# Kernel optimization log

Measured on AMD Instinct MI355X. Metric: run time of the kernel, lower is better.

## Reference

```python
import jax, jax.numpy as jnp
import numpy as np
from jax import lax

T, B, K, H, L = 256, 64, 1024, 1024, 3

def setup_inputs() -> dict:
    key = jax.random.key(0)
    ks = jax.random.split(key, 6)
    x = jax.random.normal(ks[0], (T, B, K), dtype=jnp.float32)
    h0 = jax.random.normal(ks[1], (L, B, H), dtype=jnp.float32) * 0.1
    # xavier-ish / orthogonal-ish scale for stability
    w_ih = jax.random.normal(ks[2], (L, 3 * H, K), dtype=jnp.float32) * (1.0 / np.sqrt(K))
    w_hh = jax.random.normal(ks[3], (L, 3 * H, H), dtype=jnp.float32) * (1.0 / np.sqrt(H))
    b_ih = jnp.zeros((L, 3 * H), dtype=jnp.float32)
    b_hh = jnp.zeros((L, 3 * H), dtype=jnp.float32)
    return {"x": x, "h0": h0, "w_ih": w_ih, "w_hh": w_hh, "b_ih": b_ih, "b_hh": b_hh}

def _gru_layer(x_seq, h_init, wih, whh, bih, bhh):
    # x_seq: [T,B,Kin], h_init: [B,H], wih: [3H,Kin], whh: [3H,H]
    Hd = h_init.shape[-1]
    # precompute input-to-hidden projections for all timesteps in one GEMM
    gi = jnp.einsum('tbk,gk->tbg', x_seq, wih) + bih  # [T,B,3H]

    def step(h, gi_t):
        gh = h @ whh.T + bhh  # [B,3H]
        r = jax.nn.sigmoid(gi_t[:, :Hd] + gh[:, :Hd])
        z = jax.nn.sigmoid(gi_t[:, Hd:2 * Hd] + gh[:, Hd:2 * Hd])
        n = jnp.tanh(gi_t[:, 2 * Hd:] + r * gh[:, 2 * Hd:])
        h_new = (1.0 - z) * n + z * h
        return h_new, h_new

    h_last, outs = lax.scan(step, h_init, gi)
    return h_last, outs  # [B,H], [T,B,H]

def reference(x, h0, w_ih, w_hh, b_ih, b_hh):
    layer_in = x
    h_n = []
    for l in range(w_ih.shape[0]):
        h_last, layer_in = _gru_layer(layer_in, h0[l], w_ih[l], w_hh[l], b_ih[l], b_hh[l])
        h_n.append(h_last)
    return jnp.stack(h_n, axis=0)  # [L,B,H]
```

## Files before the change

kernel.cpp:

```cpp
#include <hip/hip_runtime.h>
#include <hip/hip_bf16.h>

typedef __attribute__((ext_vector_type(8))) short bf16x8;
typedef __attribute__((ext_vector_type(4))) float f32x4;

#define T_STEPS 256
#define BATCH   64
#define KDIM    1024
#define HDIM    1024
#define NGATE   3072
#define LAYERS  3
#define SLOTE   (BATCH * HDIM)
#define RING_SLOTS (T_STEPS + 1)
#define WSZ     (192L * 32 * 64 * 8)
#define FSTRIDE 4

#define LDS_BS_BYTES  65536
#define LDS_WIS_BYTES 65536
#define GI_PAR_FLOATS (3 * 64 * 20)
#define LDS_GI_BYTES  (2 * GI_PAR_FLOATS * 4)
#define LDS_CTRL_OFF  (LDS_BS_BYTES + LDS_WIS_BYTES + LDS_GI_BYTES)
#define LDS_TOTAL     (LDS_CTRL_OFF + 32)

#define MFMA16(a, b, c) __builtin_amdgcn_mfma_f32_16x16x32_bf16(a, b, c, 0, 0, 0)

__device__ __forceinline__ unsigned short f2b(float f) {
  union { float f; unsigned int u; } a; a.f = f;
  unsigned int u = a.u;
  unsigned int r = (u + 0x7FFFu + ((u >> 16) & 1u)) >> 16;
  return (unsigned short)r;
}
__device__ __forceinline__ void gload16(const void* gptr, void* ldsptr) {
  __builtin_amdgcn_global_load_lds(
      (const __attribute__((address_space(1))) unsigned int*)gptr,
      (__attribute__((address_space(3))) unsigned int*)ldsptr,
      16, 0, 0);
}

__global__ void f2b_kernel(const float* __restrict__ src,
                           unsigned short* __restrict__ dst, int n4) {
  int i = blockIdx.x * blockDim.x + threadIdx.x;
  if (i < n4) {
    float4 v = ((const float4*)src)[i];
    ushort4 o;
    o.x = f2b(v.x); o.y = f2b(v.y); o.z = f2b(v.z); o.w = f2b(v.w);
    ((ushort4*)dst)[i] = o;
  }
}

__global__ void swizzle_w(const float* __restrict__ w,
                          unsigned short* __restrict__ out) {
  long gid = (long)blockIdx.x * 256 + threadIdx.x;
  int lane = (int)(gid & 63);
  long rest = gid >> 6;
  int kc = (int)(rest & 31); rest >>= 5;
  int ntile = (int)(rest % 192); int l = (int)(rest / 192);
  int n  = ntile * 16 + (lane & 15);
  int k0 = kc * 32 + (lane >> 4) * 8;
  const float* src = w + (((long)l * NGATE + n) * KDIM + k0);
  unsigned short o[8];
#pragma unroll
  for (int j = 0; j < 8; j++) o[j] = f2b(src[j]);
  bf16x8 v = *(bf16x8*)o;
  *(bf16x8*)(out + gid * 8) = v;
}

__global__ __launch_bounds__(512, 2) void gru_fused(
    const unsigned short* __restrict__ xb,
    const unsigned short* __restrict__ wswhh,
    const unsigned short* __restrict__ wswih,
    const float* __restrict__ bih,
    const float* __restrict__ bhh,
    const float* __restrict__ h0,
    unsigned short* __restrict__ rings,
    float* __restrict__ hout,
    unsigned int* __restrict__ flags)
{
  extern __shared__ __align__(16) char smem[];
  unsigned short* Bs  = (unsigned short*)smem;
  unsigned short* Wis = (unsigned short*)(smem + LDS_BS_BYTES);
  float* gi_lds = (float*)(smem + LDS_BS_BYTES + LDS_WIS_BYTES);
  unsigned int* ctrl = (unsigned int*)(smem + LDS_CTRL_OFF);

  int l = blockIdx.x >> 6, g = blockIdx.x & 63;
  int tid = threadIdx.x, wave = tid >> 6, lane = tid & 63;
  int lg = lane >> 4;
  int rg = wave & 3;
  bool is_h = (wave < 4);
  int row = rg * 16 + (lane & 15);
  int cb  = g * 16 + lg * 4;

  const unsigned short* whh_l = wswhh + (size_t)l * WSZ;
  const unsigned short* wih_l = wswih + (size_t)l * WSZ;
  unsigned short* ring_l = rings + (size_t)l * RING_SLOTS * SLOTE;
  const unsigned short* prev_ring = rings + (size_t)(l - 1) * RING_SLOTS * SLOTE;
  unsigned int* fl = flags + (size_t)l * 64 * FSTRIDE;
  const unsigned int* fp = flags + (size_t)(l > 0 ? (l - 1) : 0) * 64 * FSTRIDE;

  if (tid < 8) ctrl[tid] = 0;

#pragma unroll
  for (int i = 0; i < 16; i++) {
    int p = wave * 16 + i;
    int gate = (p >> 5) & 1;
    int kc = p & 31;
    const unsigned short* src = (p < 64)
        ? whh_l + ((((long)gate * 64 + g) * 32 + kc) * 64 + lane) * 8
        : wih_l + ((((long)gate * 64 + g) * 32 + kc) * 64 + lane) * 8;
    unsigned short* dst = (p < 64)
        ? &Bs[(size_t)p * 512 + (size_t)lane * 8]
        : &Wis[(size_t)(p - 64) * 512 + (size_t)lane * 8];
    gload16(src, dst);
  }

  bf16x8 wn[32];
  {
    const unsigned short* base = is_h ? whh_l : wih_l;
#pragma unroll
    for (int kc = 0; kc < 32; kc++)
      wn[kc] = *(const bf16x8*)(base + ((((long)(2 * 64 + g)) * 32 + kc) * 64 + lane) * 8);
  }

  float br_[4], bz_[4], bi_n[4], bh_n[4];
  float h[4] = {0.f, 0.f, 0.f, 0.f};
  if (is_h) {
    const float* bh_l = bhh + l * NGATE;
    const float* bi_l = bih + l * NGATE;
    float4 bhr4 = *(const float4*)(bh_l + 0 * HDIM + cb);
    float4 bhz4 = *(const float4*)(bh_l + 1 * HDIM + cb);
    float4 bhn4 = *(const float4*)(bh_l + 2 * HDIM + cb);
    float4 bir4 = *(const float4*)(bi_l + 0 * HDIM + cb);
    float4 biz4 = *(const float4*)(bi_l + 1 * HDIM + cb);
    float4 bin4 = *(const float4*)(bi_l + 2 * HDIM + cb);
    br_[0] = bir4.x + bhr4.x; br_[1] = bir4.y + bhr4.y; br_[2] = bir4.z + bhr4.z; br_[3] = bir4.w + bhr4.w;
    bz_[0] = biz4.x + bhz4.x; bz_[1] = biz4.y + bhz4.y; bz_[2] = biz4.z + bhz4.z; bz_[3] = biz4.w + bhz4.w;
    bi_n[0] = bin4.x; bi_n[1] = bin4.y; bi_n[2] = bin4.z; bi_n[3] = bin4.w;
    bh_n[0] = bhn4.x; bh_n[1] = bhn4.y; bh_n[2] = bhn4.z; bh_n[3] = bhn4.w;

    float4 h4 = *(const float4*)(h0 + (size_t)l * SLOTE + (size_t)row * HDIM + cb);
    h[0] = h4.x; h[1] = h4.y; h[2] = h4.z; h[3] = h4.w;
    union { unsigned short us[4]; unsigned long long u; } pk;
#pragma unroll
    for (int r = 0; r < 4; r++) pk.us[r] = f2b(h[r]);
    unsigned short* slotT = ring_l + (size_t)T_STEPS * SLOTE;
    __hip_atomic_store((unsigned long long*)(slotT + (size_t)g * 1024 + (size_t)row * 16 + lg * 4),
                       pk.u, __ATOMIC_RELAXED, __HIP_MEMORY_SCOPE_AGENT);
  }

  auto xgemv = [&](int tt) {
    f32x4 air = {}, aiz = {}, ain = {};
    if (l == 0) {
      const unsigned short* xa_b = xb + (size_t)tt * SLOTE + (size_t)row * KDIM + lg * 8;
#pragma unroll
      for (int kb = 0; kb < 4; kb++) {
        bf16x8 xa[8];
#pragma unroll
        for (int j = 0; j < 8; j++)
          xa[j] = *(const bf16x8*)(xa_b + (size_t)(kb * 8 + j) * 32);
#pragma unroll
        for (int j = 0; j < 8; j++) {
          int kc = kb * 8 + j;
          bf16x8 wir = *(const bf16x8*)&Wis[(size_t)kc * 512 + (size_t)lane * 8];
          bf16x8 wiz = *(const bf16x8*)&Wis[(size_t)(32 + kc) * 512 + (size_t)lane * 8];
          air = MFMA16(wir, xa[j], air);
          aiz = MFMA16(wiz, xa[j], aiz);
          ain = MFMA16(wn[kc], xa[j], ain);
        }
      }
    } else {
      const unsigned short* xa_b = prev_ring + (size_t)(T_STEPS - 1 - tt) * SLOTE
                                   + (size_t)(lg >> 1) * 1024 + (size_t)row * 16 + (lg & 1) * 8;
#pragma unroll
      for (int kb = 0; kb < 4; kb++) {
        bf16x8 xa[8];
#pragma unroll
        for (int j = 0; j < 8; j++)
          xa[j] = *(const bf16x8*)(xa_b + (size_t)(kb * 8 + j) * 2048);
#pragma unroll
        for (int j = 0; j < 8; j++) {
          int kc = kb * 8 + j;
          bf16x8 wir = *(const bf16x8*)&Wis[(size_t)kc * 512 + (size_t)lane * 8];
          bf16x8 wiz = *(const bf16x8*)&Wis[(size_t)(32 + kc) * 512 + (size_t)lane * 8];
          air = MFMA16(wir, xa[j], air);
          aiz = MFMA16(wiz, xa[j], aiz);
          ain = MFMA16(wn[kc], xa[j], ain);
        }
      }
    }
    unsigned tgt = 4u * (unsigned)(tt >> 1);
    while (__hip_atomic_load(&ctrl[3 + (tt & 1)], __ATOMIC_ACQUIRE,
                             __HIP_MEMORY_SCOPE_WORKGROUP) < tgt) {}
    float* gp = gi_lds + (size_t)(tt & 1) * GI_PAR_FLOATS + (size_t)row * 20 + lg * 4;
    *(f32x4*)(gp + 0)    = air;
    *(f32x4*)(gp + 1280) = aiz;
    *(f32x4*)(gp + 2560) = ain;
    if (lane == 0)
      __hip_atomic_fetch_add(&ctrl[1 + (tt & 1)], 1u, __ATOMIC_RELEASE,
                             __HIP_MEMORY_SCOPE_WORKGROUP);
  };

  __syncthreads();
  if (tid == 0)
    __hip_atomic_store(&fl[g * FSTRIDE], 1u, __ATOMIC_RELAXED, __HIP_MEMORY_SCOPE_AGENT);

  if (is_h) {
    while (__hip_atomic_load(&fl[lane * FSTRIDE], __ATOMIC_RELAXED,
                             __HIP_MEMORY_SCOPE_AGENT) < 1u) {}
    asm volatile("" ::: "memory");
  } else {
    if (l > 0) {
      while (__hip_atomic_load(&fp[lane * FSTRIDE], __ATOMIC_RELAXED,
                               __HIP_MEMORY_SCOPE_AGENT) < 2u) {}
      asm volatile("" ::: "memory");
    }
    xgemv(0);
  }

#pragma unroll 1
  for (int t = 0; t < T_STEPS; t++) {
    if (is_h) {
      while (__hip_atomic_load(&ctrl[1 + (t & 1)], __ATOMIC_ACQUIRE,
                               __HIP_MEMORY_SCOPE_WORKGROUP)
             < 4u * (unsigned)((t >> 1) + 1)) {}
      const float* gp = gi_lds + (size_t)(t & 1) * GI_PAR_FLOATS + (size_t)row * 20 + lg * 4;
      f32x4 xir = *(const f32x4*)(gp + 0);
      f32x4 xiz = *(const f32x4*)(gp + 1280);
      f32x4 xin = *(const f32x4*)(gp + 2560);
      asm volatile("s_waitcnt lgkmcnt(0)" ::: "memory");
      __builtin_amdgcn_sched_barrier(0);
      if (lane == 0)
        __hip_atomic_fetch_add(&ctrl[3 + (t & 1)], 1u, __ATOMIC_RELEASE,
                               __HIP_MEMORY_SCOPE_WORKGROUP);

      const unsigned short* ha_b = ring_l + (size_t)(T_STEPS - t) * SLOTE
                                   + (size_t)(lg >> 1) * 1024 + (size_t)row * 16 + (lg & 1) * 8;
      f32x4 ahr = {}, ahz = {}, ahn = {};
#pragma unroll
      for (int kb = 0; kb < 4; kb++) {
        bf16x8 hh[8];
#pragma unroll
        for (int j = 0; j < 8; j++)
          hh[j] = *(const bf16x8*)(ha_b + (size_t)(kb * 8 + j) * 2048);
#pragma unroll
        for (int j = 0; j < 8; j++) {
          int kc = kb * 8 + j;
          bf16x8 whr = *(const bf16x8*)&Bs[(size_t)kc * 512 + (size_t)lane * 8];
          bf16x8 whz = *(const bf16x8*)&Bs[(size_t)(32 + kc) * 512 + (size_t)lane * 8];
          ahr = MFMA16(whr, hh[j], ahr);
          ahz = MFMA16(whz, hh[j], ahz);
          ahn = MFMA16(wn[kc], hh[j], ahn);
        }
      }

      unsigned short* hn = ring_l + (size_t)(T_STEPS - 1 - t) * SLOTE;
      union { unsigned short us[4]; unsigned long long u; } pk;
#pragma unroll
      for (int r = 0; r < 4; r++) {
        float xr = xir[r] + ahr[r] + br_[r];
        float xz = xiz[r] + ahz[r] + bz_[r];
        float rr = 1.0f / (1.0f + __expf(-xr));
        float zz = 1.0f / (1.0f + __expf(-xz));
        float xn = (xin[r] + bi_n[r]) + rr * (ahn[r] + bh_n[r]);
        float e2 = __expf(-2.0f * xn);
        float nn = (1.0f - e2) / (1.0f + e2);
        float hv = (1.0f - zz) * nn + zz * h[r];
        h[r] = hv;
        pk.us[r] = f2b(hv);
      }
      __hip_atomic_store((unsigned long long*)(hn + (size_t)g * 1024 + (size_t)row * 16 + lg * 4),
                         pk.u, __ATOMIC_RELAXED, __HIP_MEMORY_SCOPE_AGENT);
      if (t == T_STEPS - 1) {
        float4 o; o.x = h[0]; o.y = h[1]; o.z = h[2]; o.w = h[3];
        *(float4*)(hout + (size_t)l * SLOTE + (size_t)row * HDIM + cb) = o;
      }

      asm volatile("s_waitcnt vmcnt(0)" ::: "memory");
      if (lane == 0)
        __hip_atomic_fetch_add(&ctrl[0], 1u, __ATOMIC_RELEASE,
                               __HIP_MEMORY_SCOPE_WORKGROUP);
      if (wave == 0) {
        while (__hip_atomic_load(&ctrl[0], __ATOMIC_ACQUIRE,
                                 __HIP_MEMORY_SCOPE_WORKGROUP)
               < 4u * (unsigned)(t + 1)) {}
        asm volatile("" ::: "memory");
        if (tid == 0)
          __hip_atomic_store(&fl[g * FSTRIDE], (unsigned)(t + 2),
                             __ATOMIC_RELAXED, __HIP_MEMORY_SCOPE_AGENT);
      }
      if (t + 1 < T_STEPS) {
        while (__hip_atomic_load(&fl[lane * FSTRIDE], __ATOMIC_RELAXED,
                                 __HIP_MEMORY_SCOPE_AGENT) < (unsigned)(t + 2)) {}
        asm volatile("" ::: "memory");
      }
    } else if (t + 1 < T_STEPS) {
      if (l > 0) {
        while (__hip_atomic_load(&fp[lane * FSTRIDE], __ATOMIC_RELAXED,
                                 __HIP_MEMORY_SCOPE_AGENT) < (unsigned)(t + 3)) {}
        asm volatile("" ::: "memory");
      }
      xgemv(t + 1);
    }
  }
}

extern "C" void kernel_launch(void* const* d_in, const int* in_sizes, int n_in,
                              void* d_out, int out_size, void* d_ws, size_t ws_size,
                              hipStream_t stream) {
  const float* x   = (const float*)d_in[0];
  const float* h0  = (const float*)d_in[1];
  const float* wih = (const float*)d_in[2];
  const float* whh = (const float*)d_in[3];
  const float* bih = (const float*)d_in[4];
  const float* bhh = (const float*)d_in[5];
  float* out = (float*)d_out;

  char* p = (char*)d_ws;
  unsigned short* xb    = (unsigned short*)p; p += (size_t)T_STEPS * SLOTE * 2;
  unsigned short* wswhh = (unsigned short*)p; p += (size_t)LAYERS * WSZ * 2;
  unsigned short* wswih = (unsigned short*)p; p += (size_t)LAYERS * WSZ * 2;
  unsigned short* rings = (unsigned short*)p; p += (size_t)LAYERS * RING_SLOTS * SLOTE * 2;
  unsigned int*   flags = (unsigned int*)p;   p += 4096;

  static int attr_set = 0;
  if (!attr_set) {
    hipFuncSetAttribute((const void*)gru_fused,
                        hipFuncAttributeMaxDynamicSharedMemorySize, LDS_TOTAL);
    attr_set = 1;
  }

  hipMemsetAsync(flags, 0, 4096, stream);
  f2b_kernel<<<16384, 256, 0, stream>>>(x, xb, (T_STEPS * SLOTE) / 4);
  swizzle_w<<<4608, 256, 0, stream>>>(whh, wswhh);
  swizzle_w<<<4608, 256, 0, stream>>>(wih, wswih);

  gru_fused<<<LAYERS * 64, 512, LDS_TOTAL, stream>>>(
      xb, wswhh, wswih, bih, bhh, h0, rings, out, flags);
}
```

Baseline: 2.739 ms.

## Split batch into two independent half-streams to overlap cross-block sync with compute

The batch of 64 is split into two independent 32-row halves, each with its own ring buffer, flags and LDS gate-input double buffers. Each block drops from 512 to 256 threads: two h-waves process both halves in turn and two x-waves compute input projections for both halves. While one half waits on the grid-wide flag barrier, the other half's recurrent GEMV can proceed, which is meant to hide the per-timestep global synchronization latency. In exchange each block has half the waves, so the serial work per wave doubles, and there are twice as many flags to poll.

```diff
diff --git a/kernel.cpp b/kernel.cpp
--- a/kernel.cpp
+++ b/kernel.cpp
@@ -11,16 +11,17 @@
 #define NGATE   3072
 #define LAYERS  3
 #define SLOTE   (BATCH * HDIM)
+#define HSLOTE  (32 * 1024)
 #define RING_SLOTS (T_STEPS + 1)
 #define WSZ     (192L * 32 * 64 * 8)
 #define FSTRIDE 4
 
 #define LDS_BS_BYTES  65536
 #define LDS_WIS_BYTES 65536
-#define GI_PAR_FLOATS (3 * 64 * 20)
-#define LDS_GI_BYTES  (2 * GI_PAR_FLOATS * 4)
+#define GI_BUF_FLOATS (3 * 32 * 20)
+#define LDS_GI_BYTES  (4 * GI_BUF_FLOATS * 4)
 #define LDS_CTRL_OFF  (LDS_BS_BYTES + LDS_WIS_BYTES + LDS_GI_BYTES)
-#define LDS_TOTAL     (LDS_CTRL_OFF + 32)
+#define LDS_TOTAL     (LDS_CTRL_OFF + 64)
 
 #define MFMA16(a, b, c) __builtin_amdgcn_mfma_f32_16x16x32_bf16(a, b, c, 0, 0, 0)
 
@@ -65,7 +66,7 @@
   *(bf16x8*)(out + gid * 8) = v;
 }
 
-__global__ __launch_bounds__(512, 2) void gru_fused(
+__global__ __launch_bounds__(256, 1) void gru_fused(
     const unsigned short* __restrict__ xb,
     const unsigned short* __restrict__ wswhh,
     const unsigned short* __restrict__ wswih,
@@ -85,23 +86,30 @@
   int l = blockIdx.x >> 6, g = blockIdx.x & 63;
   int tid = threadIdx.x, wave = tid >> 6, lane = tid & 63;
   int lg = lane >> 4;
-  int rg = wave & 3;
-  bool is_h = (wave < 4);
-  int row = rg * 16 + (lane & 15);
-  int cb  = g * 16 + lg * 4;
+  bool is_h = (wave < 2);
+  int w = is_h ? wave : wave - 2;
+  int rh = w * 16 + (lane & 15);
+  int cb = g * 16 + lg * 4;
 
   const unsigned short* whh_l = wswhh + (size_t)l * WSZ;
   const unsigned short* wih_l = wswih + (size_t)l * WSZ;
-  unsigned short* ring_l = rings + (size_t)l * RING_SLOTS * SLOTE;
-  const unsigned short* prev_ring = rings + (size_t)(l - 1) * RING_SLOTS * SLOTE;
-  unsigned int* fl = flags + (size_t)l * 64 * FSTRIDE;
-  const unsigned int* fp = flags + (size_t)(l > 0 ? (l - 1) : 0) * 64 * FSTRIDE;
-
-  if (tid < 8) ctrl[tid] = 0;
-
-#pragma unroll
-  for (int i = 0; i < 16; i++) {
-    int p = wave * 16 + i;
+  unsigned short* ring_m[2];
+  const unsigned short* prev_m[2];
+  unsigned int* fl_m[2];
+  const unsigned int* fp_m[2];
+#pragma unroll
+  for (int m = 0; m < 2; m++) {
+    ring_m[m] = rings + (size_t)(l * 2 + m) * RING_SLOTS * HSLOTE;
+    prev_m[m] = rings + (size_t)((l > 0 ? l - 1 : 0) * 2 + m) * RING_SLOTS * HSLOTE;
+    fl_m[m] = flags + (size_t)(l * 2 + m) * 64 * FSTRIDE;
+    fp_m[m] = flags + (size_t)((l > 0 ? l - 1 : 0) * 2 + m) * 64 * FSTRIDE;
+  }
+
+  if (tid < 16) ctrl[tid] = 0;
+
+#pragma unroll
+  for (int i = 0; i < 32; i++) {
+    int p = wave + i * 4;
     int gate = (p >> 5) & 1;
     int kc = p & 31;
     const unsigned short* src = (p < 64)
@@ -122,7 +130,7 @@
   }
 
   float br_[4], bz_[4], bi_n[4], bh_n[4];
-  float h[4] = {0.f, 0.f, 0.f, 0.f};
+  float hS[2][4];
   if (is_h) {
     const float* bh_l = bhh + l * NGATE;
     const float* bi_l = bih + l * NGATE;
@@ -136,21 +144,23 @@
     bz_[0] = biz4.x + bhz4.x; bz_[1] = biz4.y + bhz4.y; bz_[2] = biz4.z + bhz4.z; bz_[3] = biz4.w + bhz4.w;
     bi_n[0] = bin4.x; bi_n[1] = bin4.y; bi_n[2] = bin4.z; bi_n[3] = bin4.w;
     bh_n[0] = bhn4.x; bh_n[1] = bhn4.y; bh_n[2] = bhn4.z; bh_n[3] = bhn4.w;
-
-    float4 h4 = *(const float4*)(h0 + (size_t)l * SLOTE + (size_t)row * HDIM + cb);
-    h[0] = h4.x; h[1] = h4.y; h[2] = h4.z; h[3] = h4.w;
-    union { unsigned short us[4]; unsigned long long u; } pk;
-#pragma unroll
-    for (int r = 0; r < 4; r++) pk.us[r] = f2b(h[r]);
-    unsigned short* slotT = ring_l + (size_t)T_STEPS * SLOTE;
-    __hip_atomic_store((unsigned long long*)(slotT + (size_t)g * 1024 + (size_t)row * 16 + lg * 4),
-                       pk.u, __ATOMIC_RELAXED, __HIP_MEMORY_SCOPE_AGENT);
-  }
-
-  auto xgemv = [&](int tt) {
+#pragma unroll
+    for (int m = 0; m < 2; m++) {
+      float4 h4 = *(const float4*)(h0 + (size_t)l * SLOTE + (size_t)(m * 32 + rh) * HDIM + cb);
+      hS[m][0] = h4.x; hS[m][1] = h4.y; hS[m][2] = h4.z; hS[m][3] = h4.w;
+      union { unsigned short us[4]; unsigned long long u; } pk;
+#pragma unroll
+      for (int r = 0; r < 4; r++) pk.us[r] = f2b(hS[m][r]);
+      unsigned short* slotT = ring_m[m] + (size_t)T_STEPS * HSLOTE;
+      __hip_atomic_store((unsigned long long*)(slotT + (size_t)g * 512 + (size_t)rh * 16 + lg * 4),
+                         pk.u, __ATOMIC_RELAXED, __HIP_MEMORY_SCOPE_AGENT);
+    }
+  }
+
+  auto xgemv = [&](int m, int tt) {
     f32x4 air = {}, aiz = {}, ain = {};
     if (l == 0) {
-      const unsigned short* xa_b = xb + (size_t)tt * SLOTE + (size_t)row * KDIM + lg * 8;
+      const unsigned short* xa_b = xb + (size_t)tt * SLOTE + (size_t)(m * 32 + rh) * KDIM + lg * 8;
 #pragma unroll
       for (int kb = 0; kb < 4; kb++) {
         bf16x8 xa[8];
@@ -168,14 +178,14 @@
         }
       }
     } else {
-      const unsigned short* xa_b = prev_ring + (size_t)(T_STEPS - 1 - tt) * SLOTE
-                                   + (size_t)(lg >> 1) * 1024 + (size_t)row * 16 + (lg & 1) * 8;
+      const unsigned short* xa_b = prev_m[m] + (size_t)(T_STEPS - 1 - tt) * HSLOTE
+                                   + (size_t)(lg >> 1) * 512 + (size_t)rh * 16 + (lg & 1) * 8;
 #pragma unroll
       for (int kb = 0; kb < 4; kb++) {
         bf16x8 xa[8];
 #pragma unroll
         for (int j = 0; j < 8; j++)
-          xa[j] = *(const bf16x8*)(xa_b + (size_t)(kb * 8 + j) * 2048);
+          xa[j] = *(const bf16x8*)(xa_b + (size_t)(kb * 8 + j) * 1024);
 #pragma unroll
         for (int j = 0; j < 8; j++) {
           int kc = kb * 8 + j;
@@ -187,118 +197,130 @@
         }
       }
     }
-    unsigned tgt = 4u * (unsigned)(tt >> 1);
-    while (__hip_atomic_load(&ctrl[3 + (tt & 1)], __ATOMIC_ACQUIRE,
-                             __HIP_MEMORY_SCOPE_WORKGROUP) < tgt) {}
-    float* gp = gi_lds + (size_t)(tt & 1) * GI_PAR_FLOATS + (size_t)row * 20 + lg * 4;
+    int p = tt & 1;
+    while (__hip_atomic_load(&ctrl[6 + m * 2 + p], __ATOMIC_ACQUIRE,
+                             __HIP_MEMORY_SCOPE_WORKGROUP) < 2u * (unsigned)(tt >> 1)) {}
+    float* gp = gi_lds + (size_t)(m * 2 + p) * GI_BUF_FLOATS + (size_t)rh * 20 + lg * 4;
     *(f32x4*)(gp + 0)    = air;
-    *(f32x4*)(gp + 1280) = aiz;
-    *(f32x4*)(gp + 2560) = ain;
+    *(f32x4*)(gp + 640)  = aiz;
+    *(f32x4*)(gp + 1280) = ain;
     if (lane == 0)
-      __hip_atomic_fetch_add(&ctrl[1 + (tt & 1)], 1u, __ATOMIC_RELEASE,
+      __hip_atomic_fetch_add(&ctrl[2 + m * 2 + p], 1u, __ATOMIC_RELEASE,
                              __HIP_MEMORY_SCOPE_WORKGROUP);
   };
 
   __syncthreads();
-  if (tid == 0)
-    __hip_atomic_store(&fl[g * FSTRIDE], 1u, __ATOMIC_RELAXED, __HIP_MEMORY_SCOPE_AGENT);
+  if (tid == 0) {
+    __hip_atomic_store(&fl_m[0][g * FSTRIDE], 1u, __ATOMIC_RELAXED, __HIP_MEMORY_SCOPE_AGENT);
+    __hip_atomic_store(&fl_m[1][g * FSTRIDE], 1u, __ATOMIC_RELAXED, __HIP_MEMORY_SCOPE_AGENT);
+  }
 
   if (is_h) {
-    while (__hip_atomic_load(&fl[lane * FSTRIDE], __ATOMIC_RELAXED,
-                             __HIP_MEMORY_SCOPE_AGENT) < 1u) {}
+#pragma unroll
+    for (int m = 0; m < 2; m++) {
+      while (__hip_atomic_load(&fl_m[m][lane * FSTRIDE], __ATOMIC_RELAXED,
+                               __HIP_MEMORY_SCOPE_AGENT) < 1u) {}
+    }
     asm volatile("" ::: "memory");
   } else {
     if (l > 0) {
-      while (__hip_atomic_load(&fp[lane * FSTRIDE], __ATOMIC_RELAXED,
-                               __HIP_MEMORY_SCOPE_AGENT) < 2u) {}
+#pragma unroll
+      for (int m = 0; m < 2; m++) {
+        while (__hip_atomic_load(&fp_m[m][lane * FSTRIDE], __ATOMIC_RELAXED,
+                                 __HIP_MEMORY_SCOPE_AGENT) < 2u) {}
+      }
       asm volatile("" ::: "memory");
     }
-    xgemv(0);
-  }
+    xgemv(0, 0);
+    xgemv(1, 0);
+  }
+
+  auto hsub = [&](int m, int t) {
+    if (t > 0) {
+      while (__hip_atomic_load(&fl_m[m][lane * FSTRIDE], __ATOMIC_RELAXED,
+                               __HIP_MEMORY_SCOPE_AGENT) < (unsigned)(t + 1)) {}
+      asm volatile("" ::: "memory");
+    }
+    const unsigned short* ha_b = ring_m[m] + (size_t)(T_STEPS - t) * HSLOTE
+                                 + (size_t)(lg >> 1) * 512 + (size_t)rh * 16 + (lg & 1) * 8;
+    bf16x8 ha[32];
+#pragma unroll
+    for (int kc = 0; kc < 32; kc++)
+      ha[kc] = *(const bf16x8*)(ha_b + (size_t)kc * 1024);
+
+    int p = t & 1;
+    while (__hip_atomic_load(&ctrl[2 + m * 2 + p], __ATOMIC_ACQUIRE,
+                             __HIP_MEMORY_SCOPE_WORKGROUP) < 2u * (unsigned)((t >> 1) + 1)) {}
+    const float* gp = gi_lds + (size_t)(m * 2 + p) * GI_BUF_FLOATS + (size_t)rh * 20 + lg * 4;
+    f32x4 xir = *(const f32x4*)(gp + 0);
+    f32x4 xiz = *(const f32x4*)(gp + 640);
+    f32x4 xin = *(const f32x4*)(gp + 1280);
+    asm volatile("s_waitcnt lgkmcnt(0)" ::: "memory");
+    __builtin_amdgcn_sched_barrier(0);
+    if (lane == 0)
+      __hip_atomic_fetch_add(&ctrl[6 + m * 2 + p], 1u, __ATOMIC_RELEASE,
+                             __HIP_MEMORY_SCOPE_WORKGROUP);
+
+    f32x4 ahr = {}, ahz = {}, ahn = {};
+#pragma unroll
+    for (int kc = 0; kc < 32; kc++) {
+      bf16x8 whr = *(const bf16x8*)&Bs[(size_t)kc * 512 + (size_t)lane * 8];
+      bf16x8 whz = *(const bf16x8*)&Bs[(size_t)(32 + kc) * 512 + (size_t)lane * 8];
+      ahr = MFMA16(whr, ha[kc], ahr);
+      ahz = MFMA16(whz, ha[kc], ahz);
+      ahn = MFMA16(wn[kc], ha[kc], ahn);
+    }
+
+    unsigned short* hn = ring_m[m] + (size_t)(T_STEPS - 1 - t) * HSLOTE;
+    union { unsigned short us[4]; unsigned long long u; } pk;
+#pragma unroll
+    for (int r = 0; r < 4; r++) {
+      float xr = xir[r] + ahr[r] + br_[r];
+      float xz = xiz[r] + ahz[r] + bz_[r];
+      float rr = 1.0f / (1.0f + __expf(-xr));
+      float zz = 1.0f / (1.0f + __expf(-xz));
+      float xn = (xin[r] + bi_n[r]) + rr * (ahn[r] + bh_n[r]);
+      float e2 = __expf(-2.0f * xn);
+      float nn = (1.0f - e2) / (1.0f + e2);
+      float hv = (1.0f - zz) * nn + zz * hS[m][r];
+      hS[m][r] = hv;
+      pk.us[r] = f2b(hv);
+    }
+    __hip_atomic_store((unsigned long long*)(hn + (size_t)g * 512 + (size_t)rh * 16 + lg * 4),
+                       pk.u, __ATOMIC_RELAXED, __HIP_MEMORY_SCOPE_AGENT);
+    if (t == T_STEPS - 1) {
+      float4 o; o.x = hS[m][0]; o.y = hS[m][1]; o.z = hS[m][2]; o.w = hS[m][3];
+      *(float4*)(hout + (size_t)l * SLOTE + (size_t)(m * 32 + rh) * HDIM + cb) = o;
+    }
+
+    asm volatile("s_waitcnt vmcnt(0)" ::: "memory");
+    if (lane == 0)
+      __hip_atomic_fetch_add(&ctrl[m], 1u, __ATOMIC_RELEASE, __HIP_MEMORY_SCOPE_WORKGROUP);
+    if (w == 0) {
+      while (__hip_atomic_load(&ctrl[m], __ATOMIC_ACQUIRE,
+                               __HIP_MEMORY_SCOPE_WORKGROUP) < 2u * (unsigned)(t + 1)) {}
+      asm volatile("" ::: "memory");
+      if (lane == 0)
+        __hip_atomic_store(&fl_m[m][g * FSTRIDE], (unsigned)(t + 2),
+                           __ATOMIC_RELAXED, __HIP_MEMORY_SCOPE_AGENT);
+    }
+  };
 
 #pragma unroll 1
   for (int t = 0; t < T_STEPS; t++) {
     if (is_h) {
-      while (__hip_atomic_load(&ctrl[1 + (t & 1)], __ATOMIC_ACQUIRE,
-                               __HIP_MEMORY_SCOPE_WORKGROUP)
-             < 4u * (unsigned)((t >> 1) + 1)) {}
-      const float* gp = gi_lds + (size_t)(t & 1) * GI_PAR_FLOATS + (size_t)row * 20 + lg * 4;
-      f32x4 xir = *(const f32x4*)(gp + 0);
-      f32x4 xiz = *(const f32x4*)(gp + 1280);
-      f32x4 xin = *(const f32x4*)(gp + 2560);
-      asm volatile("s_waitcnt lgkmcnt(0)" ::: "memory");
-      __builtin_amdgcn_sched_barrier(0);
-      if (lane == 0)
-        __hip_atomic_fetch_add(&ctrl[3 + (t & 1)], 1u, __ATOMIC_RELEASE,
-                               __HIP_MEMORY_SCOPE_WORKGROUP);
-
-      const unsigned short* ha_b = ring_l + (size_t)(T_STEPS - t) * SLOTE
-                                   + (size_t)(lg >> 1) * 1024 + (size_t)row * 16 + (lg & 1) * 8;
-      f32x4 ahr = {}, ahz = {}, ahn = {};
-#pragma unroll
-      for (int kb = 0; kb < 4; kb++) {
-        bf16x8 hh[8];
-#pragma unroll
-        for (int j = 0; j < 8; j++)
-          hh[j] = *(const bf16x8*)(ha_b + (size_t)(kb * 8 + j) * 2048);
-#pragma unroll
-        for (int j = 0; j < 8; j++) {
-          int kc = kb * 8 + j;
-          bf16x8 whr = *(const bf16x8*)&Bs[(size_t)kc * 512 + (size_t)lane * 8];
-          bf16x8 whz = *(const bf16x8*)&Bs[(size_t)(32 + kc) * 512 + (size_t)lane * 8];
-          ahr = MFMA16(whr, hh[j], ahr);
-          ahz = MFMA16(whz, hh[j], ahz);
-          ahn = MFMA16(wn[kc], hh[j], ahn);
+      hsub(0, t);
+      hsub(1, t);
+    } else if (t + 1 < T_STEPS) {
+#pragma unroll
+      for (int m = 0; m < 2; m++) {
+        if (l > 0) {
+          while (__hip_atomic_load(&fp_m[m][lane * FSTRIDE], __ATOMIC_RELAXED,
+                                   __HIP_MEMORY_SCOPE_AGENT) < (unsigned)(t + 3)) {}
+          asm volatile("" ::: "memory");
         }
+        xgemv(m, t + 1);
       }
-
-      unsigned short* hn = ring_l + (size_t)(T_STEPS - 1 - t) * SLOTE;
-      union { unsigned short us[4]; unsigned long long u; } pk;
-#pragma unroll
-      for (int r = 0; r < 4; r++) {
-        float xr = xir[r] + ahr[r] + br_[r];
-        float xz = xiz[r] + ahz[r] + bz_[r];
-        float rr = 1.0f / (1.0f + __expf(-xr));
-        float zz = 1.0f / (1.0f + __expf(-xz));
-        float xn = (xin[r] + bi_n[r]) + rr * (ahn[r] + bh_n[r]);
-        float e2 = __expf(-2.0f * xn);
-        float nn = (1.0f - e2) / (1.0f + e2);
-        float hv = (1.0f - zz) * nn + zz * h[r];
-        h[r] = hv;
-        pk.us[r] = f2b(hv);
-      }
-      __hip_atomic_store((unsigned long long*)(hn + (size_t)g * 1024 + (size_t)row * 16 + lg * 4),
-                         pk.u, __ATOMIC_RELAXED, __HIP_MEMORY_SCOPE_AGENT);
-      if (t == T_STEPS - 1) {
-        float4 o; o.x = h[0]; o.y = h[1]; o.z = h[2]; o.w = h[3];
-        *(float4*)(hout + (size_t)l * SLOTE + (size_t)row * HDIM + cb) = o;
-      }
-
-      asm volatile("s_waitcnt vmcnt(0)" ::: "memory");
-      if (lane == 0)
-        __hip_atomic_fetch_add(&ctrl[0], 1u, __ATOMIC_RELEASE,
-                               __HIP_MEMORY_SCOPE_WORKGROUP);
-      if (wave == 0) {
-        while (__hip_atomic_load(&ctrl[0], __ATOMIC_ACQUIRE,
-                                 __HIP_MEMORY_SCOPE_WORKGROUP)
-               < 4u * (unsigned)(t + 1)) {}
-        asm volatile("" ::: "memory");
-        if (tid == 0)
-          __hip_atomic_store(&fl[g * FSTRIDE], (unsigned)(t + 2),
-                             __ATOMIC_RELAXED, __HIP_MEMORY_SCOPE_AGENT);
-      }
-      if (t + 1 < T_STEPS) {
-        while (__hip_atomic_load(&fl[lane * FSTRIDE], __ATOMIC_RELAXED,
-                                 __HIP_MEMORY_SCOPE_AGENT) < (unsigned)(t + 2)) {}
-        asm volatile("" ::: "memory");
-      }
-    } else if (t + 1 < T_STEPS) {
-      if (l > 0) {
-        while (__hip_atomic_load(&fp[lane * FSTRIDE], __ATOMIC_RELAXED,
-                                 __HIP_MEMORY_SCOPE_AGENT) < (unsigned)(t + 3)) {}
-        asm volatile("" ::: "memory");
-      }
-      xgemv(t + 1);
     }
   }
 }
@@ -318,8 +340,8 @@
   unsigned short* xb    = (unsigned short*)p; p += (size_t)T_STEPS * SLOTE * 2;
   unsigned short* wswhh = (unsigned short*)p; p += (size_t)LAYERS * WSZ * 2;
   unsigned short* wswih = (unsigned short*)p; p += (size_t)LAYERS * WSZ * 2;
-  unsigned short* rings = (unsigned short*)p; p += (size_t)LAYERS * RING_SLOTS * SLOTE * 2;
-  unsigned int*   flags = (unsigned int*)p;   p += 4096;
+  unsigned short* rings = (unsigned short*)p; p += (size_t)LAYERS * 2 * RING_SLOTS * HSLOTE * 2;
+  unsigned int*   flags = (unsigned int*)p;   p += 8192;
 
   static int attr_set = 0;
   if (!attr_set) {
@@ -328,11 +350,11 @@
     attr_set = 1;
   }
 
-  hipMemsetAsync(flags, 0, 4096, stream);
+  hipMemsetAsync(flags, 0, 8192, stream);
   f2b_kernel<<<16384, 256, 0, stream>>>(x, xb, (T_STEPS * SLOTE) / 4);
   swizzle_w<<<4608, 256, 0, stream>>>(whh, wswhh);
   swizzle_w<<<4608, 256, 0, stream>>>(wih, wswih);
 
-  gru_fused<<<LAYERS * 64, 512, LDS_TOTAL, stream>>>(
+  gru_fused<<<LAYERS * 64, 256, LDS_TOTAL, stream>>>(
       xb, wswhh, wswih, bih, bhh, h0, rings, out, flags);
 }
```

Result: slower. 3.497 ms (+27.7%).

## Halve workgroup to 4 waves, each wave computing two 16-row tiles

Applied to the files above, without the earlier changes.

The fused GRU workgroup shrinks from 8 waves to 4: two recurrent waves and two input-projection waves, each covering two 16-row batch tiles so LDS weight fragments and the register-resident n-gate weights are reused across both tiles. The cross-workgroup flag wait moves to the top of the step, overlapping the spin with the gi handoff, and the ring loads for the whole K range are issued up front. This cuts LDS weight reads per MFMA and barrier participants per step, at the cost of higher register pressure (64 bf16x8 hidden fragments plus 32 weight fragments) and less latency hiding from fewer waves.

```diff
diff --git a/kernel.cpp b/kernel.cpp
--- a/kernel.cpp
+++ b/kernel.cpp
@@ -20,7 +20,7 @@
 #define GI_PAR_FLOATS (3 * 64 * 20)
 #define LDS_GI_BYTES  (2 * GI_PAR_FLOATS * 4)
 #define LDS_CTRL_OFF  (LDS_BS_BYTES + LDS_WIS_BYTES + LDS_GI_BYTES)
-#define LDS_TOTAL     (LDS_CTRL_OFF + 32)
+#define LDS_TOTAL     (LDS_CTRL_OFF + 64)
 
 #define MFMA16(a, b, c) __builtin_amdgcn_mfma_f32_16x16x32_bf16(a, b, c, 0, 0, 0)
 
@@ -65,7 +65,7 @@
   *(bf16x8*)(out + gid * 8) = v;
 }
 
-__global__ __launch_bounds__(512, 2) void gru_fused(
+__global__ __launch_bounds__(256, 1) void gru_fused(
     const unsigned short* __restrict__ xb,
     const unsigned short* __restrict__ wswhh,
     const unsigned short* __restrict__ wswih,
@@ -85,10 +85,11 @@
   int l = blockIdx.x >> 6, g = blockIdx.x & 63;
   int tid = threadIdx.x, wave = tid >> 6, lane = tid & 63;
   int lg = lane >> 4;
-  int rg = wave & 3;
-  bool is_h = (wave < 4);
-  int row = rg * 16 + (lane & 15);
-  int cb  = g * 16 + lg * 4;
+  bool is_h = (wave < 2);
+  int w = is_h ? wave : wave - 2;
+  int row0 = w * 16 + (lane & 15);
+  int row1 = 32 + row0;
+  int cb = g * 16 + lg * 4;
 
   const unsigned short* whh_l = wswhh + (size_t)l * WSZ;
   const unsigned short* wih_l = wswih + (size_t)l * WSZ;
@@ -97,11 +98,11 @@
   unsigned int* fl = flags + (size_t)l * 64 * FSTRIDE;
   const unsigned int* fp = flags + (size_t)(l > 0 ? (l - 1) : 0) * 64 * FSTRIDE;
 
-  if (tid < 8) ctrl[tid] = 0;
-
-#pragma unroll
-  for (int i = 0; i < 16; i++) {
-    int p = wave * 16 + i;
+  if (tid < 16) ctrl[tid] = 0;
+
+#pragma unroll
+  for (int i = 0; i < 32; i++) {
+    int p = wave + i * 4;
     int gate = (p >> 5) & 1;
     int kc = p & 31;
     const unsigned short* src = (p < 64)
@@ -122,7 +123,7 @@
   }
 
   float br_[4], bz_[4], bi_n[4], bh_n[4];
-  float h[4] = {0.f, 0.f, 0.f, 0.f};
+  float hS[2][4];
   if (is_h) {
     const float* bh_l = bhh + l * NGATE;
     const float* bi_l = bih + l * NGATE;
@@ -136,66 +137,63 @@
     bz_[0] = biz4.x + bhz4.x; bz_[1] = biz4.y + bhz4.y; bz_[2] = biz4.z + bhz4.z; bz_[3] = biz4.w + bhz4.w;
     bi_n[0] = bin4.x; bi_n[1] = bin4.y; bi_n[2] = bin4.z; bi_n[3] = bin4.w;
     bh_n[0] = bhn4.x; bh_n[1] = bhn4.y; bh_n[2] = bhn4.z; bh_n[3] = bhn4.w;
-
-    float4 h4 = *(const float4*)(h0 + (size_t)l * SLOTE + (size_t)row * HDIM + cb);
-    h[0] = h4.x; h[1] = h4.y; h[2] = h4.z; h[3] = h4.w;
-    union { unsigned short us[4]; unsigned long long u; } pk;
-#pragma unroll
-    for (int r = 0; r < 4; r++) pk.us[r] = f2b(h[r]);
     unsigned short* slotT = ring_l + (size_t)T_STEPS * SLOTE;
-    __hip_atomic_store((unsigned long long*)(slotT + (size_t)g * 1024 + (size_t)row * 16 + lg * 4),
-                       pk.u, __ATOMIC_RELAXED, __HIP_MEMORY_SCOPE_AGENT);
+#pragma unroll
+    for (int rt = 0; rt < 2; rt++) {
+      int row = rt ? row1 : row0;
+      float4 h4 = *(const float4*)(h0 + (size_t)l * SLOTE + (size_t)row * HDIM + cb);
+      hS[rt][0] = h4.x; hS[rt][1] = h4.y; hS[rt][2] = h4.z; hS[rt][3] = h4.w;
+      union { unsigned short us[4]; unsigned long long u; } pk;
+#pragma unroll
+      for (int r = 0; r < 4; r++) pk.us[r] = f2b(hS[rt][r]);
+      __hip_atomic_store((unsigned long long*)(slotT + (size_t)g * 1024 + (size_t)row * 16 + lg * 4),
+                         pk.u, __ATOMIC_RELAXED, __HIP_MEMORY_SCOPE_AGENT);
+    }
   }
 
   auto xgemv = [&](int tt) {
-    f32x4 air = {}, aiz = {}, ain = {};
-    if (l == 0) {
-      const unsigned short* xa_b = xb + (size_t)tt * SLOTE + (size_t)row * KDIM + lg * 8;
-#pragma unroll
-      for (int kb = 0; kb < 4; kb++) {
-        bf16x8 xa[8];
-#pragma unroll
-        for (int j = 0; j < 8; j++)
-          xa[j] = *(const bf16x8*)(xa_b + (size_t)(kb * 8 + j) * 32);
-#pragma unroll
-        for (int j = 0; j < 8; j++) {
-          int kc = kb * 8 + j;
-          bf16x8 wir = *(const bf16x8*)&Wis[(size_t)kc * 512 + (size_t)lane * 8];
-          bf16x8 wiz = *(const bf16x8*)&Wis[(size_t)(32 + kc) * 512 + (size_t)lane * 8];
-          air = MFMA16(wir, xa[j], air);
-          aiz = MFMA16(wiz, xa[j], aiz);
-          ain = MFMA16(wn[kc], xa[j], ain);
-        }
-      }
-    } else {
-      const unsigned short* xa_b = prev_ring + (size_t)(T_STEPS - 1 - tt) * SLOTE
-                                   + (size_t)(lg >> 1) * 1024 + (size_t)row * 16 + (lg & 1) * 8;
-#pragma unroll
-      for (int kb = 0; kb < 4; kb++) {
-        bf16x8 xa[8];
-#pragma unroll
-        for (int j = 0; j < 8; j++)
-          xa[j] = *(const bf16x8*)(xa_b + (size_t)(kb * 8 + j) * 2048);
-#pragma unroll
-        for (int j = 0; j < 8; j++) {
-          int kc = kb * 8 + j;
-          bf16x8 wir = *(const bf16x8*)&Wis[(size_t)kc * 512 + (size_t)lane * 8];
-          bf16x8 wiz = *(const bf16x8*)&Wis[(size_t)(32 + kc) * 512 + (size_t)lane * 8];
-          air = MFMA16(wir, xa[j], air);
-          aiz = MFMA16(wiz, xa[j], aiz);
-          ain = MFMA16(wn[kc], xa[j], ain);
-        }
-      }
-    }
-    unsigned tgt = 4u * (unsigned)(tt >> 1);
-    while (__hip_atomic_load(&ctrl[3 + (tt & 1)], __ATOMIC_ACQUIRE,
-                             __HIP_MEMORY_SCOPE_WORKGROUP) < tgt) {}
-    float* gp = gi_lds + (size_t)(tt & 1) * GI_PAR_FLOATS + (size_t)row * 20 + lg * 4;
-    *(f32x4*)(gp + 0)    = air;
-    *(f32x4*)(gp + 1280) = aiz;
-    *(f32x4*)(gp + 2560) = ain;
+    int p = tt & 1;
+    float* gbase = gi_lds + (size_t)p * GI_PAR_FLOATS;
+    f32x4 acc[2][3];
+#pragma unroll
+    for (int rt = 0; rt < 2; rt++) {
+      int row = rt ? row1 : row0;
+      f32x4 air = {}, aiz = {}, ain = {};
+      bf16x8 xa[32];
+      if (l == 0) {
+        const unsigned short* xa_b = xb + (size_t)tt * SLOTE + (size_t)row * KDIM + lg * 8;
+#pragma unroll
+        for (int kc = 0; kc < 32; kc++)
+          xa[kc] = *(const bf16x8*)(xa_b + (size_t)kc * 32);
+      } else {
+        const unsigned short* xa_b = prev_ring + (size_t)(T_STEPS - 1 - tt) * SLOTE
+                                     + (size_t)(lg >> 1) * 1024 + (size_t)row * 16 + (lg & 1) * 8;
+#pragma unroll
+        for (int kc = 0; kc < 32; kc++)
+          xa[kc] = *(const bf16x8*)(xa_b + (size_t)kc * 2048);
+      }
+#pragma unroll
+      for (int kc = 0; kc < 32; kc++) {
+        bf16x8 wir = *(const bf16x8*)&Wis[(size_t)kc * 512 + (size_t)lane * 8];
+        bf16x8 wiz = *(const bf16x8*)&Wis[(size_t)(32 + kc) * 512 + (size_t)lane * 8];
+        air = MFMA16(wir, xa[kc], air);
+        aiz = MFMA16(wiz, xa[kc], aiz);
+        ain = MFMA16(wn[kc], xa[kc], ain);
+      }
+      acc[rt][0] = air; acc[rt][1] = aiz; acc[rt][2] = ain;
+    }
+    while (__hip_atomic_load(&ctrl[4 + p], __ATOMIC_ACQUIRE,
+                             __HIP_MEMORY_SCOPE_WORKGROUP) < 2u * (unsigned)(tt >> 1)) {}
+#pragma unroll
+    for (int rt = 0; rt < 2; rt++) {
+      int row = rt ? row1 : row0;
+      float* gp = gbase + (size_t)row * 20 + lg * 4;
+      *(f32x4*)(gp + 0)    = acc[rt][0];
+      *(f32x4*)(gp + 1280) = acc[rt][1];
+      *(f32x4*)(gp + 2560) = acc[rt][2];
+    }
     if (lane == 0)
-      __hip_atomic_fetch_add(&ctrl[1 + (tt & 1)], 1u, __ATOMIC_RELEASE,
+      __hip_atomic_fetch_add(&ctrl[2 + p], 1u, __ATOMIC_RELEASE,
                              __HIP_MEMORY_SCOPE_WORKGROUP);
   };
 
@@ -219,78 +217,88 @@
 #pragma unroll 1
   for (int t = 0; t < T_STEPS; t++) {
     if (is_h) {
-      while (__hip_atomic_load(&ctrl[1 + (t & 1)], __ATOMIC_ACQUIRE,
-                               __HIP_MEMORY_SCOPE_WORKGROUP)
-             < 4u * (unsigned)((t >> 1) + 1)) {}
-      const float* gp = gi_lds + (size_t)(t & 1) * GI_PAR_FLOATS + (size_t)row * 20 + lg * 4;
-      f32x4 xir = *(const f32x4*)(gp + 0);
-      f32x4 xiz = *(const f32x4*)(gp + 1280);
-      f32x4 xin = *(const f32x4*)(gp + 2560);
+      if (t > 0) {
+        while (__hip_atomic_load(&fl[lane * FSTRIDE], __ATOMIC_RELAXED,
+                                 __HIP_MEMORY_SCOPE_AGENT) < (unsigned)(t + 1)) {}
+        asm volatile("" ::: "memory");
+      }
+      const unsigned short* slot = ring_l + (size_t)(T_STEPS - t) * SLOTE;
+      const unsigned short* ha_b0 = slot + (size_t)(lg >> 1) * 1024 + (size_t)row0 * 16 + (lg & 1) * 8;
+      const unsigned short* ha_b1 = slot + (size_t)(lg >> 1) * 1024 + (size_t)row1 * 16 + (lg & 1) * 8;
+      bf16x8 ha0[32], ha1[32];
+#pragma unroll
+      for (int kc = 0; kc < 32; kc++) ha0[kc] = *(const bf16x8*)(ha_b0 + (size_t)kc * 2048);
+#pragma unroll
+      for (int kc = 0; kc < 32; kc++) ha1[kc] = *(const bf16x8*)(ha_b1 + (size_t)kc * 2048);
+
+      int p = t & 1;
+      while (__hip_atomic_load(&ctrl[2 + p], __ATOMIC_ACQUIRE,
+                               __HIP_MEMORY_SCOPE_WORKGROUP) < 2u * (unsigned)((t >> 1) + 1)) {}
+      const float* gbase = gi_lds + (size_t)p * GI_PAR_FLOATS;
+      f32x4 xi[2][3];
+#pragma unroll
+      for (int rt = 0; rt < 2; rt++) {
+        const float* gp = gbase + (size_t)(rt ? row1 : row0) * 20 + lg * 4;
+        xi[rt][0] = *(const f32x4*)(gp + 0);
+        xi[rt][1] = *(const f32x4*)(gp + 1280);
+        xi[rt][2] = *(const f32x4*)(gp + 2560);
+      }
       asm volatile("s_waitcnt lgkmcnt(0)" ::: "memory");
       __builtin_amdgcn_sched_barrier(0);
       if (lane == 0)
-        __hip_atomic_fetch_add(&ctrl[3 + (t & 1)], 1u, __ATOMIC_RELEASE,
+        __hip_atomic_fetch_add(&ctrl[4 + p], 1u, __ATOMIC_RELEASE,
                                __HIP_MEMORY_SCOPE_WORKGROUP);
 
-      const unsigned short* ha_b = ring_l + (size_t)(T_STEPS - t) * SLOTE
-                                   + (size_t)(lg >> 1) * 1024 + (size_t)row * 16 + (lg & 1) * 8;
-      f32x4 ahr = {}, ahz = {}, ahn = {};
-#pragma unroll
-      for (int kb = 0; kb < 4; kb++) {
-        bf16x8 hh[8];
-#pragma unroll
-        for (int j = 0; j < 8; j++)
-          hh[j] = *(const bf16x8*)(ha_b + (size_t)(kb * 8 + j) * 2048);
-#pragma unroll
-        for (int j = 0; j < 8; j++) {
-          int kc = kb * 8 + j;
-          bf16x8 whr = *(const bf16x8*)&Bs[(size_t)kc * 512 + (size_t)lane * 8];
-          bf16x8 whz = *(const bf16x8*)&Bs[(size_t)(32 + kc) * 512 + (size_t)lane * 8];
-          ahr = MFMA16(whr, hh[j], ahr);
-          ahz = MFMA16(whz, hh[j], ahz);
-          ahn = MFMA16(wn[kc], hh[j], ahn);
+      f32x4 ar0 = {}, az0 = {}, an0 = {}, ar1 = {}, az1 = {}, an1 = {};
+#pragma unroll
+      for (int kc = 0; kc < 32; kc++) {
+        bf16x8 whr = *(const bf16x8*)&Bs[(size_t)kc * 512 + (size_t)lane * 8];
+        bf16x8 whz = *(const bf16x8*)&Bs[(size_t)(32 + kc) * 512 + (size_t)lane * 8];
+        ar0 = MFMA16(whr, ha0[kc], ar0);
+        az0 = MFMA16(whz, ha0[kc], az0);
+        an0 = MFMA16(wn[kc], ha0[kc], an0);
+        ar1 = MFMA16(whr, ha1[kc], ar1);
+        az1 = MFMA16(whz, ha1[kc], az1);
+        an1 = MFMA16(wn[kc], ha1[kc], an1);
+      }
+
+      unsigned short* hn = ring_l + (size_t)(T_STEPS - 1 - t) * SLOTE;
+#pragma unroll
+      for (int rt = 0; rt < 2; rt++) {
+        f32x4 ahr = rt ? ar1 : ar0, ahz = rt ? az1 : az0, ahn = rt ? an1 : an0;
+        int row = rt ? row1 : row0;
+        union { unsigned short us[4]; unsigned long long u; } pk;
+#pragma unroll
+        for (int r = 0; r < 4; r++) {
+          float xr = xi[rt][0][r] + ahr[r] + br_[r];
+          float xz = xi[rt][1][r] + ahz[r] + bz_[r];
+          float rr = 1.0f / (1.0f + __expf(-xr));
+          float zz = 1.0f / (1.0f + __expf(-xz));
+          float xn = (xi[rt][2][r] + bi_n[r]) + rr * (ahn[r] + bh_n[r]);
+          float e2 = __expf(-2.0f * xn);
+          float nn = (1.0f - e2) / (1.0f + e2);
+          float hv = (1.0f - zz) * nn + zz * hS[rt][r];
+          hS[rt][r] = hv;
+          pk.us[r] = f2b(hv);
         }
-      }
-
-      unsigned short* hn = ring_l + (size_t)(T_STEPS - 1 - t) * SLOTE;
-      union { unsigned short us[4]; unsigned long long u; } pk;
-#pragma unroll
-      for (int r = 0; r < 4; r++) {
-        float xr = xir[r] + ahr[r] + br_[r];
-        float xz = xiz[r] + ahz[r] + bz_[r];
-        float rr = 1.0f / (1.0f + __expf(-xr));
-        float zz = 1.0f / (1.0f + __expf(-xz));
-        float xn = (xin[r] + bi_n[r]) + rr * (ahn[r] + bh_n[r]);
-        float e2 = __expf(-2.0f * xn);
-        float nn = (1.0f - e2) / (1.0f + e2);
-        float hv = (1.0f - zz) * nn + zz * h[r];
-        h[r] = hv;
-        pk.us[r] = f2b(hv);
-      }
-      __hip_atomic_store((unsigned long long*)(hn + (size_t)g * 1024 + (size_t)row * 16 + lg * 4),
-                         pk.u, __ATOMIC_RELAXED, __HIP_MEMORY_SCOPE_AGENT);
-      if (t == T_STEPS - 1) {
-        float4 o; o.x = h[0]; o.y = h[1]; o.z = h[2]; o.w = h[3];
-        *(float4*)(hout + (size_t)l * SLOTE + (size_t)row * HDIM + cb) = o;
+        __hip_atomic_store((unsigned long long*)(hn + (size_t)g * 1024 + (size_t)row * 16 + lg * 4),
+                           pk.u, __ATOMIC_RELAXED, __HIP_MEMORY_SCOPE_AGENT);
+        if (t == T_STEPS - 1) {
+          float4 o; o.x = hS[rt][0]; o.y = hS[rt][1]; o.z = hS[rt][2]; o.w = hS[rt][3];
+          *(float4*)(hout + (size_t)l * SLOTE + (size_t)row * HDIM + cb) = o;
+        }
       }
 
       asm volatile("s_waitcnt vmcnt(0)" ::: "memory");
       if (lane == 0)
-        __hip_atomic_fetch_add(&ctrl[0], 1u, __ATOMIC_RELEASE,
-                               __HIP_MEMORY_SCOPE_WORKGROUP);
-      if (wave == 0) {
+        __hip_atomic_fetch_add(&ctrl[0], 1u, __ATOMIC_RELEASE, __HIP_MEMORY_SCOPE_WORKGROUP);
+      if (w == 0) {
         while (__hip_atomic_load(&ctrl[0], __ATOMIC_ACQUIRE,
-                                 __HIP_MEMORY_SCOPE_WORKGROUP)
-               < 4u * (unsigned)(t + 1)) {}
+                                 __HIP_MEMORY_SCOPE_WORKGROUP) < 2u * (unsigned)(t + 1)) {}
         asm volatile("" ::: "memory");
-        if (tid == 0)
+        if (lane == 0)
           __hip_atomic_store(&fl[g * FSTRIDE], (unsigned)(t + 2),
                              __ATOMIC_RELAXED, __HIP_MEMORY_SCOPE_AGENT);
-      }
-      if (t + 1 < T_STEPS) {
-        while (__hip_atomic_load(&fl[lane * FSTRIDE], __ATOMIC_RELAXED,
-                                 __HIP_MEMORY_SCOPE_AGENT) < (unsigned)(t + 2)) {}
-        asm volatile("" ::: "memory");
       }
     } else if (t + 1 < T_STEPS) {
       if (l > 0) {
@@ -333,6 +341,6 @@
   swizzle_w<<<4608, 256, 0, stream>>>(whh, wswhh);
   swizzle_w<<<4608, 256, 0, stream>>>(wih, wswih);
 
-  gru_fused<<<LAYERS * 64, 512, LDS_TOTAL, stream>>>(
+  gru_fused<<<LAYERS * 64, 256, LDS_TOTAL, stream>>>(
       xb, wswhh, wswih, bih, bhh, h0, rings, out, flags);
 }
```

New measurement: 3.908 ms. 42.7% more time.
